# Kernel optimization log

Measured on AMD Instinct MI355X. Metric: run time of the kernel, lower is better.

## Reference

```python
import jax, jax.numpy as jnp
import numpy as np

TAU = 0.05
BETA = 8.0
MAX_ITERS = 6
EPS = 1e-12  # torch F.normalize eps


def setup_inputs() -> dict:
    key = jax.random.key(0)
    P, d, C, h = 20000, 128, 512, 4
    k1, k2, k3, k4 = jax.random.split(key, 4)
    K = jax.random.normal(k1, (P, d), dtype=jnp.float32) * 0.1
    Theta = jax.random.normal(k2, (C, d, h), dtype=jnp.float32)
    head_idx = jax.random.randint(k3, (C,), 0, P)
    initial_val = jax.random.uniform(k4, (P,), dtype=jnp.float32)
    return {"K": K, "Theta": Theta, "head_idx": head_idx, "initial_val": initial_val}


def _l2norm(x, axis):
    n = jnp.sqrt(jnp.sum(x * x, axis=axis, keepdims=True))
    return x / jnp.maximum(n, EPS)


def reference(K, Theta, head_idx, initial_val):
    P = K.shape[0]
    C, d, h = Theta.shape
    Kn = _l2norm(K, axis=1)            # [P, d]
    Thetan = _l2norm(Theta, axis=1)    # [C, d, h] (normalize over d, per slot)
    # cosine similarity per clause/slot: S[c, p, s]
    S = jnp.einsum('pd,cds->cps', Kn, Thetan)          # [C, P, h]
    best = jnp.argmax(S, axis=1)                        # [C, h] best predicate per slot
    conf = jnp.take_along_axis(S, best[:, None, :], axis=1)[:, 0, :]  # [C, h]
    beta_eff = max(BETA, 1.0)
    n = 2 * h
    log_n = jnp.float32(np.log(n))

    val = initial_val
    for _ in range(MAX_ITERS):
        vals = val[best]                                # [C, h] truth values at argmax preds
        combined = jnp.concatenate([conf, vals], axis=1)  # [C, 2h]
        # softmin_tau(x) = -(1/tau) * (logsumexp(-x/tau) - log n)
        g = -(1.0 / TAU) * (jax.nn.logsumexp(-combined / TAU, axis=1) - log_n)
        g = jnp.clip(g, 0.0, 1.0)                       # [C]
        # soft OR per head: (1/beta) * logsumexp(beta * g) over clauses sharing a head
        e = jax.ops.segment_sum(jnp.exp(beta_eff * g), head_idx, num_segments=P)
        g_head = jnp.log(jnp.maximum(e, 1e-38)) / beta_eff
        val = jnp.where(e > 0, jnp.maximum(val, g_head), val)
    return val
```

## Files before the change

kernel.cpp:

```cpp
#include <hip/hip_runtime.h>
#include <hip/hip_bf16.h>
#include <math.h>

#define D_DIM 128
#define H_DIM 4

typedef __attribute__((ext_vector_type(4))) float f32x4;
typedef __attribute__((ext_vector_type(8))) __bf16 bf16x8v;

__device__ inline unsigned int f2bf(float f) {
    __hip_bfloat16 b = __float2bfloat16(f);
    return (unsigned int)*reinterpret_cast<unsigned short*>(&b);
}
__device__ inline unsigned int encf(float v) {
    unsigned int u = __float_as_uint(v);
    return (u & 0x80000000u) ? ~u : (u | 0x80000000u);
}
__device__ inline float decf(unsigned int ub) {
    unsigned int fb = (ub & 0x80000000u) ? (ub ^ 0x80000000u) : ~ub;
    return __uint_as_float(fb);
}

__global__ __launch_bounds__(256) void k_prep(
    const float* __restrict__ K, unsigned int* __restrict__ Knb,
    float* __restrict__ rnK,
    const float* __restrict__ Theta, unsigned int* __restrict__ Tnb,
    float* __restrict__ Tn32,
    const float* __restrict__ initial, float* __restrict__ out,
    int* __restrict__ head_of, int P, int Ppad, int NJ)
{
    int wave = threadIdx.x >> 6, lane = threadIdx.x & 63;
    int row = blockIdx.x * 4 + wave;
    if (row < Ppad) {
        if (row >= P) {
            Knb[(size_t)row * 64 + lane] = 0u;
        } else {
            float2 v = ((const float2*)(K + (size_t)row * D_DIM))[lane];
            float ss = v.x * v.x + v.y * v.y;
            #pragma unroll
            for (int off = 1; off < 64; off <<= 1) ss += __shfl_xor(ss, off);
            float rn = 1.0f / fmaxf(sqrtf(ss), 1e-12f);
            Knb[(size_t)row * 64 + lane] = f2bf(v.x * rn) | (f2bf(v.y * rn) << 16);
            if (lane == 0) {
                rnK[row] = rn;
                out[row] = initial[row];
                head_of[row] = 0x7FFFFFFF;
            }
        }
    }
    if (blockIdx.x < (NJ >> 2)) {
        int j = blockIdx.x * 4 + wave;
        int c = j >> 2, s = j & 3;
        const float* base = Theta + (size_t)c * (D_DIM * H_DIM) + s;
        float t0 = base[(2 * lane) * H_DIM];
        float t1 = base[(2 * lane + 1) * H_DIM];
        float ss = t0 * t0 + t1 * t1;
        #pragma unroll
        for (int off = 1; off < 64; off <<= 1) ss += __shfl_xor(ss, off);
        float rn = 1.0f / fmaxf(sqrtf(ss), 1e-12f);
        float n0 = t0 * rn, n1 = t1 * rn;
        Tnb[(size_t)j * 64 + lane] = f2bf(n0) | (f2bf(n1) << 16);
        float2 w; w.x = n0; w.y = n1;
        ((float2*)(Tn32 + (size_t)j * D_DIM))[lane] = w;
    }
}

__global__ __launch_bounds__(256) void k_fused2(
    const unsigned short* __restrict__ Knb, const unsigned short* __restrict__ Tnb,
    const float* __restrict__ K, const float* __restrict__ rnK,
    const float* __restrict__ Tn32,
    unsigned int* __restrict__ gmax, unsigned long long* __restrict__ cand,
    int P, int NBLK)
{
    __shared__ __align__(16) unsigned short As[128 * 128];
    __shared__ __align__(16) unsigned short Bs[128 * 128];
    __shared__ int queue[512];
    __shared__ int qn;

    int tid = threadIdx.x;
    int lane = tid & 63;
    int wave = tid >> 6;
    if (tid == 0) qn = 0;

    int orig = blockIdx.x;
    int q8 = NBLK >> 3, r8 = NBLK & 7;
    int xcd = orig & 7, idx = orig >> 3;
    int wgid = (xcd < r8 ? xcd * (q8 + 1) : r8 * (q8 + 1) + (xcd - r8) * q8) + idx;
    int pt = wgid >> 4, jt = wgid & 15;
    int p0 = pt * 128, j0 = jt * 128;

    {
        int rr = lane >> 4, ccc = lane & 15;
        const unsigned short* gA = Tnb + (size_t)j0 * 128;
        const unsigned short* gB = Knb + (size_t)p0 * 128;
        #pragma unroll
        for (int i = 0; i < 8; i++) {
            int r0 = wave * 32 + i * 4;
            int rw = r0 + rr;
            int sc = (ccc ^ (rw & 7)) << 3;
            __builtin_amdgcn_global_load_lds(
                (const __attribute__((address_space(1))) unsigned int*)(gA + (size_t)rw * 128 + sc),
                (__attribute__((address_space(3))) unsigned int*)&As[r0 * 128], 16, 0, 0);
            __builtin_amdgcn_global_load_lds(
                (const __attribute__((address_space(1))) unsigned int*)(gB + (size_t)rw * 128 + sc),
                (__attribute__((address_space(3))) unsigned int*)&Bs[r0 * 128], 16, 0, 0);
        }
    }
    __syncthreads();

    int wm = wave >> 1, wn = wave & 1;
    int lr = lane & 15, lg = lane >> 4;
    f32x4 acc[4][4];
    #pragma unroll
    for (int m = 0; m < 4; m++)
        #pragma unroll
        for (int n = 0; n < 4; n++) { f32x4 z = {0.f, 0.f, 0.f, 0.f}; acc[m][n] = z; }
    #pragma unroll
    for (int ks = 0; ks < 4; ks++) {
        int koff = (8 * lg + 32 * ks) ^ ((lr & 7) << 3);
        bf16x8v af[4], bv[4];
        #pragma unroll
        for (int m = 0; m < 4; m++)
            af[m] = *(const bf16x8v*)&As[(64 * wm + 16 * m + lr) * 128 + koff];
        #pragma unroll
        for (int n = 0; n < 4; n++)
            bv[n] = *(const bf16x8v*)&Bs[(64 * wn + 16 * n + lr) * 128 + koff];
        #pragma unroll
        for (int m = 0; m < 4; m++)
            #pragma unroll
            for (int n = 0; n < 4; n++)
                acc[m][n] = __builtin_amdgcn_mfma_f32_16x16x32_bf16(af[m], bv[n], acc[m][n], 0, 0, 0);
    }
    __syncthreads();

    float* red = (float*)As;
    #pragma unroll
    for (int m = 0; m < 4; m++) {
        #pragma unroll
        for (int n2 = 0; n2 < 2; n2++) {
            f32x4 a0 = acc[m][2 * n2], a1 = acc[m][2 * n2 + 1];
            float t0 = fmaxf(a0[0], a1[0]);
            float t1 = fmaxf(a0[1], a1[1]);
            float t2 = fmaxf(a0[2], a1[2]);
            float t3 = fmaxf(a0[3], a1[3]);
            #pragma unroll
            for (int off = 1; off <= 8; off <<= 1) {
                t0 = fmaxf(t0, __shfl_xor(t0, off));
                t1 = fmaxf(t1, __shfl_xor(t1, off));
                t2 = fmaxf(t2, __shfl_xor(t2, off));
                t3 = fmaxf(t3, __shfl_xor(t3, off));
            }
            if (lr == 0) {
                int jb = 64 * wm + 16 * m + 4 * lg;
                int ch = 2 * wn + n2;
                red[(jb + 0) * 4 + ch] = t0;
                red[(jb + 1) * 4 + ch] = t1;
                red[(jb + 2) * 4 + ch] = t2;
                red[(jb + 3) * 4 + ch] = t3;
            }
        }
    }
    __syncthreads();

    if (tid < 128) {
        int jl = tid, j = j0 + jl;
        float tmax = fmaxf(fmaxf(red[jl * 4 + 0], red[jl * 4 + 1]),
                           fmaxf(red[jl * 4 + 2], red[jl * 4 + 3]));
        unsigned int old = atomicMax(&gmax[j], encf(tmax));
        float vmax = fmaxf(decf(old), tmax);
        float thr = vmax - 0.009f;
        #pragma unroll
        for (int ch = 0; ch < 4; ch++) {
            if (red[jl * 4 + ch] >= thr) {
                int qi = atomicAdd(&qn, 1);
                queue[qi] = jl * 4 + ch;
            }
        }
    }
    __syncthreads();

    int nq = qn;
    int half = lane & 1, pl = lane >> 1;
    for (int e = wave; e < nq; e += 4) {
        int qe = queue[e];
        int jl = qe >> 2, ch = qe & 3;
        int j = j0 + jl;
        int p = p0 + ch * 32 + pl;
        bool ok = (p < P);
        int pc = ok ? p : 0;
        const float4* kp = (const float4*)(K + (size_t)pc * D_DIM + half * 64);
        const float4* tp = (const float4*)(Tn32 + (size_t)j * D_DIM + half * 64);
        float sx = 0.f, sy = 0.f, sz = 0.f, sw = 0.f;
        #pragma unroll
        for (int k4 = 0; k4 < 16; k4++) {
            float4 a = kp[k4], bb = tp[k4];
            sx = fmaf(a.x, bb.x, sx); sy = fmaf(a.y, bb.y, sy);
            sz = fmaf(a.z, bb.z, sz); sw = fmaf(a.w, bb.w, sw);
        }
        float dot = (sx + sy) + (sz + sw);
        dot += __shfl_xor(dot, 1);
        float v = ok ? dot * rnK[pc] : -INFINITY;
        int bp = p;
        #pragma unroll
        for (int off = 2; off < 64; off <<= 1) {
            float ov = __shfl_xor(v, off);
            int op = __shfl_xor(bp, off);
            if (ov > v || (ov == v && op < bp)) { v = ov; bp = op; }
        }
        if (lane == 0) {
            unsigned long long key =
                ((unsigned long long)encf(v) << 32) | (unsigned int)(0x7FFFFFFF - bp);
            atomicMax(&cand[j], key);
        }
    }
}

__global__ __launch_bounds__(512) void k_logic2(
    const int* __restrict__ head_idx, const float* __restrict__ initial_val,
    const unsigned long long* __restrict__ cand, int* __restrict__ head_of,
    float* __restrict__ out, int C)
{
    __shared__ float hval[512];
    __shared__ float elds[512];
    int c = threadIdx.x;
    int h = head_idx[c];
    atomicMin(&head_of[h], c);
    __syncthreads();
    int myslot = __hip_atomic_load(&head_of[h], __ATOMIC_RELAXED, __HIP_MEMORY_SCOPE_AGENT);
    hval[c] = initial_val[h];

    float cf[H_DIM], v0[H_DIM]; int bs[H_DIM];
    #pragma unroll
    for (int s = 0; s < H_DIM; s++) {
        unsigned long long key = cand[c * H_DIM + s];
        cf[s] = decf((unsigned int)(key >> 32));
        int b = 0x7FFFFFFF - (int)(key & 0xFFFFFFFFu);
        v0[s] = initial_val[b];
        int ho = __hip_atomic_load(&head_of[b], __ATOMIC_RELAXED, __HIP_MEMORY_SCOPE_AGENT);
        bs[s] = (ho < C) ? ho : -1;
    }
    __syncthreads();

    const float inv_tau = 20.0f;
    const float logn = logf(2.0f * H_DIM);
    const float beta = 8.0f;

    for (int it = 0; it < 6; it++) {
        float x[2 * H_DIM];
        #pragma unroll
        for (int s = 0; s < H_DIM; s++) {
            x[s] = cf[s];
            x[H_DIM + s] = (bs[s] >= 0) ? hval[bs[s]] : v0[s];
        }
        float cur = hval[myslot];
        elds[c] = 0.f;
        __syncthreads();

        float m = x[0];
        #pragma unroll
        for (int i = 1; i < 2 * H_DIM; i++) m = fminf(m, x[i]);
        float ssum = 0.f;
        #pragma unroll
        for (int i = 0; i < 2 * H_DIM; i++) ssum += expf((m - x[i]) * inv_tau);
        float g = -inv_tau * ((-m * inv_tau + logf(ssum)) - logn);
        g = fminf(fmaxf(g, 0.f), 1.f);
        atomicAdd(&elds[myslot], expf(beta * g));
        __syncthreads();

        float e = elds[myslot];
        float gh = logf(fmaxf(e, 1e-38f)) / beta;
        float nv = fmaxf(cur, gh);
        if (myslot == c) hval[c] = nv;
        __syncthreads();
    }

    if (myslot == c) out[h] = hval[c];
}

extern "C" void kernel_launch(void* const* d_in, const int* in_sizes, int n_in,
                              void* d_out, int out_size, void* d_ws, size_t ws_size,
                              hipStream_t stream) {
    const float* K        = (const float*)d_in[0];
    const float* Theta    = (const float*)d_in[1];
    const int*   head_idx = (const int*)d_in[2];
    const float* initial  = (const float*)d_in[3];
    float* out = (float*)d_out;

    int P  = in_sizes[3];
    int C  = in_sizes[2];
    int NJ = C * H_DIM;
    int Ppad = ((P + 127) / 128) * 128;
    int NT = Ppad / 128;
    int NBLK = NT * (NJ / 128);

    char* w = (char*)d_ws;
    size_t off = 0;
    auto alloc = [&](size_t bytes) { void* p = w + off; off += (bytes + 255) & ~(size_t)255; return p; };
    unsigned int* Knb  = (unsigned int*)alloc((size_t)Ppad * D_DIM * 2);
    unsigned int* Tnb  = (unsigned int*)alloc((size_t)NJ * D_DIM * 2);
    float* Tn32 = (float*)alloc((size_t)NJ * D_DIM * 4);
    float* rnK  = (float*)alloc((size_t)P * 4);
    unsigned int* gmax       = (unsigned int*)alloc((size_t)NJ * 4);
    unsigned long long* cand = (unsigned long long*)alloc((size_t)NJ * 8);
    int* head_of             = (int*)alloc((size_t)P * 4);
    (void)ws_size; (void)n_in; (void)out_size;

    k_prep<<<Ppad / 4, 256, 0, stream>>>(K, Knb, rnK, Theta, Tnb, Tn32,
                                         initial, out, head_of, P, Ppad, NJ);
    k_fused2<<<NBLK, 256, 0, stream>>>((const unsigned short*)Knb,
                                       (const unsigned short*)Tnb,
                                       K, rnK, Tn32, gmax, cand, P, NBLK);
    k_logic2<<<1, C, 0, stream>>>(head_idx, initial, cand, head_of, out, C);
}
```

Baseline: 75.39 us.

## Make fused similarity blocks persistent over several P tiles with deferred candidate filtering

Instead of one block per 128x128 tile, each of 512 blocks keeps its Theta tile in LDS and loops over 4-5 consecutive K tiles. Per-tile partial maxima are staged in shared memory and the candidate threshold is computed only after all of the block's tiles are done, so gmax has usually absorbed more tiles before filtering. This is meant to cut the number of fp32 rescoring candidates and to reuse the A tile. In exchange there is more shared memory, less parallelism and only a partly overlapped reload of the B tile. The hardcoded split (29x5+3x4 = 157 tiles, 16 j-tiles) ties the launch to this problem size.

```diff
diff --git a/kernel.cpp b/kernel.cpp
--- a/kernel.cpp
+++ b/kernel.cpp
@@ -4,6 +4,7 @@
 
 #define D_DIM 128
 #define H_DIM 4
+#define QCAP 1024
 
 typedef __attribute__((ext_vector_type(4))) float f32x4;
 typedef __attribute__((ext_vector_type(8))) __bf16 bf16x8v;
@@ -60,44 +61,46 @@
         float rn = 1.0f / fmaxf(sqrtf(ss), 1e-12f);
         float n0 = t0 * rn, n1 = t1 * rn;
         Tnb[(size_t)j * 64 + lane] = f2bf(n0) | (f2bf(n1) << 16);
-        float2 w; w.x = n0; w.y = n1;
-        ((float2*)(Tn32 + (size_t)j * D_DIM))[lane] = w;
-    }
-}
-
-__global__ __launch_bounds__(256) void k_fused2(
+        float2 w2; w2.x = n0; w2.y = n1;
+        ((float2*)(Tn32 + (size_t)j * D_DIM))[lane] = w2;
+    }
+}
+
+__global__ __launch_bounds__(256) void k_fused3(
     const unsigned short* __restrict__ Knb, const unsigned short* __restrict__ Tnb,
     const float* __restrict__ K, const float* __restrict__ rnK,
     const float* __restrict__ Tn32,
     unsigned int* __restrict__ gmax, unsigned long long* __restrict__ cand,
-    int P, int NBLK)
+    int P)
 {
     __shared__ __align__(16) unsigned short As[128 * 128];
     __shared__ __align__(16) unsigned short Bs[128 * 128];
-    __shared__ int queue[512];
+    __shared__ float sred[5 * 512];
+    __shared__ float thrl[128];
+    __shared__ unsigned short queue[QCAP];
     __shared__ int qn;
 
-    int tid = threadIdx.x;
-    int lane = tid & 63;
-    int wave = tid >> 6;
+    const int tid = threadIdx.x;
+    const int lane = tid & 63;
+    const int wave = tid >> 6;
     if (tid == 0) qn = 0;
 
-    int orig = blockIdx.x;
-    int q8 = NBLK >> 3, r8 = NBLK & 7;
-    int xcd = orig & 7, idx = orig >> 3;
-    int wgid = (xcd < r8 ? xcd * (q8 + 1) : r8 * (q8 + 1) + (xcd - r8) * q8) + idx;
-    int pt = wgid >> 4, jt = wgid & 15;
-    int p0 = pt * 128, j0 = jt * 128;
+    const int jt = blockIdx.x >> 5;
+    const int w  = blockIdx.x & 31;
+    const int begin = (w < 29) ? w * 5 : 29 * 5 + (w - 29) * 4;
+    const int cnt   = (w < 29) ? 5 : 4;
+    const int j0 = jt * 128;
+
+    const int rr = lane >> 4, cc = lane & 15;
 
     {
-        int rr = lane >> 4, ccc = lane & 15;
         const unsigned short* gA = Tnb + (size_t)j0 * 128;
-        const unsigned short* gB = Knb + (size_t)p0 * 128;
+        const unsigned short* gB = Knb + (size_t)(begin * 128) * 128;
         #pragma unroll
         for (int i = 0; i < 8; i++) {
             int r0 = wave * 32 + i * 4;
             int rw = r0 + rr;
-            int sc = (ccc ^ (rw & 7)) << 3;
+            int sc = (cc ^ (rw & 7)) << 3;
             __builtin_amdgcn_global_load_lds(
                 (const __attribute__((address_space(1))) unsigned int*)(gA + (size_t)rw * 128 + sc),
                 (__attribute__((address_space(3))) unsigned int*)&As[r0 * 128], 16, 0, 0);
@@ -108,84 +111,111 @@
     }
     __syncthreads();
 
-    int wm = wave >> 1, wn = wave & 1;
-    int lr = lane & 15, lg = lane >> 4;
-    f32x4 acc[4][4];
-    #pragma unroll
-    for (int m = 0; m < 4; m++)
-        #pragma unroll
-        for (int n = 0; n < 4; n++) { f32x4 z = {0.f, 0.f, 0.f, 0.f}; acc[m][n] = z; }
-    #pragma unroll
-    for (int ks = 0; ks < 4; ks++) {
-        int koff = (8 * lg + 32 * ks) ^ ((lr & 7) << 3);
-        bf16x8v af[4], bv[4];
+    const int wm = wave >> 1, wn = wave & 1;
+    const int lr = lane & 15, lg = lane >> 4;
+    float runmax = -INFINITY;
+
+    for (int t = 0; t < cnt; t++) {
+        f32x4 acc[4][4];
         #pragma unroll
         for (int m = 0; m < 4; m++)
-            af[m] = *(const bf16x8v*)&As[(64 * wm + 16 * m + lr) * 128 + koff];
-        #pragma unroll
-        for (int n = 0; n < 4; n++)
-            bv[n] = *(const bf16x8v*)&Bs[(64 * wn + 16 * n + lr) * 128 + koff];
-        #pragma unroll
-        for (int m = 0; m < 4; m++)
+            #pragma unroll
+            for (int n = 0; n < 4; n++) { f32x4 z = {0.f, 0.f, 0.f, 0.f}; acc[m][n] = z; }
+        #pragma unroll
+        for (int ks = 0; ks < 4; ks++) {
+            int koff = (8 * lg + 32 * ks) ^ ((lr & 7) << 3);
+            bf16x8v af[4], bv[4];
+            #pragma unroll
+            for (int m = 0; m < 4; m++)
+                af[m] = *(const bf16x8v*)&As[(64 * wm + 16 * m + lr) * 128 + koff];
             #pragma unroll
             for (int n = 0; n < 4; n++)
-                acc[m][n] = __builtin_amdgcn_mfma_f32_16x16x32_bf16(af[m], bv[n], acc[m][n], 0, 0, 0);
-    }
-    __syncthreads();
-
-    float* red = (float*)As;
-    #pragma unroll
-    for (int m = 0; m < 4; m++) {
-        #pragma unroll
-        for (int n2 = 0; n2 < 2; n2++) {
-            f32x4 a0 = acc[m][2 * n2], a1 = acc[m][2 * n2 + 1];
-            float t0 = fmaxf(a0[0], a1[0]);
-            float t1 = fmaxf(a0[1], a1[1]);
-            float t2 = fmaxf(a0[2], a1[2]);
-            float t3 = fmaxf(a0[3], a1[3]);
-            #pragma unroll
-            for (int off = 1; off <= 8; off <<= 1) {
-                t0 = fmaxf(t0, __shfl_xor(t0, off));
-                t1 = fmaxf(t1, __shfl_xor(t1, off));
-                t2 = fmaxf(t2, __shfl_xor(t2, off));
-                t3 = fmaxf(t3, __shfl_xor(t3, off));
+                bv[n] = *(const bf16x8v*)&Bs[(64 * wn + 16 * n + lr) * 128 + koff];
+            #pragma unroll
+            for (int m = 0; m < 4; m++)
+                #pragma unroll
+                for (int n = 0; n < 4; n++)
+                    acc[m][n] = __builtin_amdgcn_mfma_f32_16x16x32_bf16(af[m], bv[n], acc[m][n], 0, 0, 0);
+        }
+        __syncthreads();
+
+        if (t + 1 < cnt) {
+            const unsigned short* gB = Knb + (size_t)((begin + t + 1) * 128) * 128;
+            #pragma unroll
+            for (int i = 0; i < 8; i++) {
+                int r0 = wave * 32 + i * 4;
+                int rw = r0 + rr;
+                int sc = (cc ^ (rw & 7)) << 3;
+                __builtin_amdgcn_global_load_lds(
+                    (const __attribute__((address_space(1))) unsigned int*)(gB + (size_t)rw * 128 + sc),
+                    (__attribute__((address_space(3))) unsigned int*)&Bs[r0 * 128], 16, 0, 0);
             }
-            if (lr == 0) {
-                int jb = 64 * wm + 16 * m + 4 * lg;
-                int ch = 2 * wn + n2;
-                red[(jb + 0) * 4 + ch] = t0;
-                red[(jb + 1) * 4 + ch] = t1;
-                red[(jb + 2) * 4 + ch] = t2;
-                red[(jb + 3) * 4 + ch] = t3;
+        }
+
+        #pragma unroll
+        for (int m = 0; m < 4; m++) {
+            #pragma unroll
+            for (int n2 = 0; n2 < 2; n2++) {
+                f32x4 a0 = acc[m][2 * n2], a1 = acc[m][2 * n2 + 1];
+                float t0 = fmaxf(a0[0], a1[0]);
+                float t1 = fmaxf(a0[1], a1[1]);
+                float t2 = fmaxf(a0[2], a1[2]);
+                float t3 = fmaxf(a0[3], a1[3]);
+                #pragma unroll
+                for (int off = 1; off <= 8; off <<= 1) {
+                    t0 = fmaxf(t0, __shfl_xor(t0, off));
+                    t1 = fmaxf(t1, __shfl_xor(t1, off));
+                    t2 = fmaxf(t2, __shfl_xor(t2, off));
+                    t3 = fmaxf(t3, __shfl_xor(t3, off));
+                }
+                if (lr == 0) {
+                    int jb = 64 * wm + 16 * m + 4 * lg;
+                    int ch = 2 * wn + n2;
+                    sred[t * 512 + (jb + 0) * 4 + ch] = t0;
+                    sred[t * 512 + (jb + 1) * 4 + ch] = t1;
+                    sred[t * 512 + (jb + 2) * 4 + ch] = t2;
+                    sred[t * 512 + (jb + 3) * 4 + ch] = t3;
+                }
             }
         }
-    }
-    __syncthreads();
+        __syncthreads();
+
+        if (tid < 128) {
+            const float* sr = &sred[t * 512 + tid * 4];
+            float tmax = fmaxf(fmaxf(sr[0], sr[1]), fmaxf(sr[2], sr[3]));
+            if (tmax > runmax) {
+                runmax = tmax;
+                atomicMax(&gmax[j0 + tid], encf(tmax));
+            }
+        }
+    }
 
     if (tid < 128) {
-        int jl = tid, j = j0 + jl;
-        float tmax = fmaxf(fmaxf(red[jl * 4 + 0], red[jl * 4 + 1]),
-                           fmaxf(red[jl * 4 + 2], red[jl * 4 + 3]));
-        unsigned int old = atomicMax(&gmax[j], encf(tmax));
-        float vmax = fmaxf(decf(old), tmax);
-        float thr = vmax - 0.009f;
-        #pragma unroll
-        for (int ch = 0; ch < 4; ch++) {
-            if (red[jl * 4 + ch] >= thr) {
-                int qi = atomicAdd(&qn, 1);
-                queue[qi] = jl * 4 + ch;
-            }
+        unsigned int gv = __hip_atomic_load(&gmax[j0 + tid], __ATOMIC_RELAXED,
+                                            __HIP_MEMORY_SCOPE_AGENT);
+        thrl[tid] = decf(gv) - 0.009f;
+    }
+    __syncthreads();
+
+    for (int e = tid; e < cnt * 512; e += 256) {
+        int jl = (e >> 2) & 127;
+        if (sred[e] >= thrl[jl]) {
+            int qi = atomicAdd(&qn, 1);
+            if (qi < QCAP) queue[qi] = (unsigned short)e;
         }
     }
     __syncthreads();
 
     int nq = qn;
+    bool ovf = (nq > QCAP);
+    int tot = ovf ? cnt * 512 : nq;
     int half = lane & 1, pl = lane >> 1;
-    for (int e = wave; e < nq; e += 4) {
-        int qe = queue[e];
-        int jl = qe >> 2, ch = qe & 3;
+    for (int i = wave; i < tot; i += 4) {
+        int e = ovf ? i : (int)queue[i];
+        int t = e >> 9, rem = e & 511;
+        int jl = rem >> 2, ch = rem & 3;
         int j = j0 + jl;
-        int p = p0 + ch * 32 + pl;
+        int p = (begin + t) * 128 + ch * 32 + pl;
         bool ok = (p < P);
         int pc = ok ? p : 0;
         const float4* kp = (const float4*)(K + (size_t)pc * D_DIM + half * 64);
@@ -290,8 +320,7 @@
     int C  = in_sizes[2];
     int NJ = C * H_DIM;
     int Ppad = ((P + 127) / 128) * 128;
-    int NT = Ppad / 128;
-    int NBLK = NT * (NJ / 128);
+    (void)ws_size; (void)n_in; (void)out_size;
 
     char* w = (char*)d_ws;
     size_t off = 0;
@@ -303,12 +332,11 @@
     unsigned int* gmax       = (unsigned int*)alloc((size_t)NJ * 4);
     unsigned long long* cand = (unsigned long long*)alloc((size_t)NJ * 8);
     int* head_of             = (int*)alloc((size_t)P * 4);
-    (void)ws_size; (void)n_in; (void)out_size;
 
     k_prep<<<Ppad / 4, 256, 0, stream>>>(K, Knb, rnK, Theta, Tnb, Tn32,
                                          initial, out, head_of, P, Ppad, NJ);
-    k_fused2<<<NBLK, 256, 0, stream>>>((const unsigned short*)Knb,
-                                       (const unsigned short*)Tnb,
-                                       K, rnK, Tn32, gmax, cand, P, NBLK);
+    k_fused3<<<512, 256, 0, stream>>>((const unsigned short*)Knb,
+                                      (const unsigned short*)Tnb,
+                                      K, rnK, Tn32, gmax, cand, P);
     k_logic2<<<1, C, 0, stream>>>(head_idx, initial, cand, head_of, out, C);
 }
```

Result: no change. 75.12 us (-0.4%).
